# Kernel tuning notes

Hardware: AMD Instinct MI355X
Metric: run time of the kernel (lower is better)

The kernel has to match this reference:

```python
import jax, jax.numpy as jnp
import numpy as np

S, B, H = 4096, 64, 256
D = 2.0
SIGMA = D / 2.0


def setup_inputs() -> dict:
    key = jax.random.key(0)
    ks = jax.random.split(key, 7)
    return {
        "e": jax.random.normal(ks[0], (S, B, H), dtype=jnp.float32),
        "d": jax.random.normal(ks[1], (1, B, H), dtype=jnp.float32),
        "W_a": jax.random.normal(ks[2], (H, H), dtype=jnp.float32) / np.sqrt(H),
        "W_p": jax.random.normal(ks[3], (H, H), dtype=jnp.float32) / np.sqrt(H),
        "v_p": jax.random.normal(ks[4], (H, 1), dtype=jnp.float32) / np.sqrt(H),
        "lin_w": jax.random.normal(ks[5], (H, 2 * H), dtype=jnp.float32) / np.sqrt(2 * H),
        "lin_b": jax.random.normal(ks[6], (H,), dtype=jnp.float32) * 0.01,
    }


def reference(e, d, W_a, W_p, v_p, lin_w, lin_b):
    s = e.shape[0]
    # alignment: scores over source positions, softmax along S (dim 0 in torch)
    scores = jnp.sum((d @ W_a) * e, axis=2)          # [S, B]
    a = jax.nn.softmax(scores, axis=0)               # [S, B]
    # predictive position gating (Luong local-p attention)
    h = jnp.tanh(d[0] @ W_p)                         # [B, H]
    p_center = jax.nn.sigmoid((h @ v_p)[:, 0])[None, :] * s   # [1, B]
    pos = jnp.arange(s, dtype=e.dtype)[:, None]      # [S, 1]
    diff = p_center - pos                            # [S, B]
    mask = (jnp.abs(diff) <= D).astype(e.dtype)
    p = jnp.exp(-(diff * diff) / (2.0 * SIGMA * SIGMA)) * mask  # [S, B]
    w = a * p                                        # [S, B]
    context = jnp.einsum('sbh,sb->bh', e, w)[None]   # [1, B, H]
    x = jnp.concatenate([context, d], axis=2)        # [1, B, 2H]
    out = jax.nn.relu(x @ lin_w.T + lin_b)           # dropout = identity (eval)
    return out, w
```

## Files before the change

### kernel.cpp

```cpp
#include <hip/hip_runtime.h>
#include <math.h>

constexpr int S_ = 4096;
constexpr int B_ = 64;
constexpr int H_ = 256;


__global__ __launch_bounds__(256) void k1_prep(const float* __restrict__ d,
                                               const float* __restrict__ W_a,
                                               const float* __restrict__ W_p,
                                               const float* __restrict__ v_p,
                                               float* __restrict__ dW,
                                               float* __restrict__ pc) {
  int b = blockIdx.x;
  int h = threadIdx.x;
  float acc_a = 0.f, acc_p = 0.f;
  const float* db = d + b * H_;
  for (int k = 0; k < H_; ++k) {
    float dv = db[k];
    acc_a = fmaf(dv, W_a[k * H_ + h], acc_a);
    acc_p = fmaf(dv, W_p[k * H_ + h], acc_p);
  }
  dW[b * H_ + h] = acc_a;
  float prod = tanhf(acc_p) * v_p[h];
  __shared__ float red[256];
  red[h] = prod;
  __syncthreads();
  for (int st = 128; st > 0; st >>= 1) {
    if (h < st) red[h] += red[h + st];
    __syncthreads();
  }
  if (h == 0) {
    pc[b] = (float)S_ / (1.f + expf(-red[0]));
  }
}

__global__ __launch_bounds__(256) void k2_scores(const float* __restrict__ e,
                                                 const float* __restrict__ dW,
                                                 float* __restrict__ scores) {
  int b = blockIdx.x;
  int wave = threadIdx.x >> 6;
  int lane = threadIdx.x & 63;
  float4 wv = *(const float4*)(dW + b * H_ + lane * 4);
  int s_base = blockIdx.y * 64 + wave * 16;
  const float* ebase = e + (size_t)s_base * (B_ * H_) + (size_t)b * H_ + (size_t)lane * 4;
#pragma unroll 1
  for (int c = 0; c < 2; ++c) {
    float4 ev[8];
#pragma unroll
    for (int i = 0; i < 8; ++i)
      ev[i] = *(const float4*)(ebase + (size_t)(c * 8 + i) * (B_ * H_));
#pragma unroll
    for (int i = 0; i < 8; ++i) {
      float acc = fmaf(ev[i].x, wv.x, fmaf(ev[i].y, wv.y, fmaf(ev[i].z, wv.z, ev[i].w * wv.w)));
#pragma unroll
      for (int off = 32; off > 0; off >>= 1) acc += __shfl_xor(acc, off, 64);
      if (lane == 0) scores[b * S_ + s_base + c * 8 + i] = acc;
    }
  }
}

__global__ __launch_bounds__(256) void kF(const float* __restrict__ scores,
                                          const float* __restrict__ pc,
                                          const float* __restrict__ e,
                                          const float* __restrict__ d,
                                          const float* __restrict__ lin_w,
                                          const float* __restrict__ lin_b,
                                          float* __restrict__ out,
                                          float* __restrict__ w_out) {
  int b = blockIdx.x;
  int t = threadIdx.x;
  const float* sc = scores + b * S_;
  float v[16];
  float lm = -INFINITY;
#pragma unroll
  for (int k = 0; k < 16; ++k) {
    v[k] = sc[t + k * 256];
    lm = fmaxf(lm, v[k]);
  }
  __shared__ float red[256];
  red[t] = lm;
  __syncthreads();
  for (int st = 128; st > 0; st >>= 1) {
    if (t < st) red[t] = fmaxf(red[t], red[t + st]);
    __syncthreads();
  }
  float mb = red[0];
  __syncthreads();
  float ls = 0.f;
#pragma unroll
  for (int k = 0; k < 16; ++k) ls += expf(v[k] - mb);
  red[t] = ls;
  __syncthreads();
  for (int st = 128; st > 0; st >>= 1) {
    if (t < st) red[t] += red[t + st];
    __syncthreads();
  }
  float inv_l = 1.f / red[0];
  float pcb = pc[b];
#pragma unroll
  for (int k = 0; k < 16; ++k) {
    int s = t + k * 256;
    float diff = pcb - (float)s;
    float p = (fabsf(diff) <= 2.f) ? expf(-0.5f * diff * diff) : 0.f;
    w_out[(size_t)s * B_ + b] = expf(v[k] - mb) * inv_l * p;
  }
  int s0 = max(0, (int)ceilf(pcb - 2.f));
  int s1 = min(S_ - 1, (int)floorf(pcb + 2.f));
  float ctx = 0.f;
  for (int s = s0; s <= s1; ++s) {
    float diff = pcb - (float)s;
    float wv = expf(sc[s] - mb) * inv_l * expf(-0.5f * diff * diff);
    ctx = fmaf(wv, e[((size_t)s * B_ + b) * H_ + t], ctx);
  }
  __shared__ float x[512];
  x[t] = ctx;
  x[256 + t] = d[b * H_ + t];
  __syncthreads();
  float acc = lin_b[t];
  const float4* lw = (const float4*)(lin_w + t * 2 * H_);
  const float4* xv = (const float4*)x;
#pragma unroll 4
  for (int k = 0; k < 128; ++k) {
    float4 a4 = lw[k];
    float4 b4 = xv[k];
    acc += a4.x * b4.x + a4.y * b4.y + a4.z * b4.z + a4.w * b4.w;
  }
  out[b * H_ + t] = fmaxf(acc, 0.f);
}

extern "C" void kernel_launch(void* const* d_in, const int* in_sizes, int n_in,
                              void* d_out, int out_size, void* d_ws, size_t ws_size,
                              hipStream_t stream) {
  const float* e     = (const float*)d_in[0];
  const float* d     = (const float*)d_in[1];
  const float* W_a   = (const float*)d_in[2];
  const float* W_p   = (const float*)d_in[3];
  const float* v_p   = (const float*)d_in[4];
  const float* lin_w = (const float*)d_in[5];
  const float* lin_b = (const float*)d_in[6];

  float* out   = (float*)d_out;
  float* w_out = out + B_ * H_;

  float* ws     = (float*)d_ws;
  float* dW     = ws;
  float* pc     = ws + 16384;
  float* scores = ws + 16448;

  k1_prep<<<B_, 256, 0, stream>>>(d, W_a, W_p, v_p, dW, pc);
  k2_scores<<<dim3(B_, S_ / 64), 256, 0, stream>>>(e, dW, scores);
  kF<<<B_, 256, 0, stream>>>(scores, pc, e, d, lin_w, lin_b, out, w_out);
}
```

Before: 83.87 us.

## Restructure score kernel so each block covers all batches for four positions

The score kernel now assigns four threads per batch row and keeps that row's dW vector in registers. Each block handles four source positions across all 64 batches and reads contiguous slabs of e. This replaces the full 64-lane shuffle reduction per row with a 2-step reduction and coalesces score writes through a shared-memory transpose. The cost is higher register use (16 float4 of weights plus 8 float4 loads in flight) and a strided access pattern within each thread's row.

Measured after the change: 86.05 us. 2.6% more time.

```diff
diff --git a/kernel.cpp b/kernel.cpp
--- a/kernel.cpp
+++ b/kernel.cpp
@@ -38,26 +38,49 @@
 __global__ __launch_bounds__(256) void k2_scores(const float* __restrict__ e,
                                                  const float* __restrict__ dW,
                                                  float* __restrict__ scores) {
-  int b = blockIdx.x;
-  int wave = threadIdx.x >> 6;
-  int lane = threadIdx.x & 63;
-  float4 wv = *(const float4*)(dW + b * H_ + lane * 4);
-  int s_base = blockIdx.y * 64 + wave * 16;
-  const float* ebase = e + (size_t)s_base * (B_ * H_) + (size_t)b * H_ + (size_t)lane * 4;
-#pragma unroll 1
-  for (int c = 0; c < 2; ++c) {
-    float4 ev[8];
+  int t = threadIdx.x;
+  int wave = t >> 6;
+  int lane = t & 63;
+  int bl = lane >> 2;
+  int sub = lane & 3;
+  int b = wave * 16 + bl;
+  int s0 = blockIdx.x * 4;
+
+  const float4* dW4 = (const float4*)(dW + b * H_);
+  float4 wreg[16];
 #pragma unroll
-    for (int i = 0; i < 8; ++i)
-      ev[i] = *(const float4*)(ebase + (size_t)(c * 8 + i) * (B_ * H_));
+  for (int j = 0; j < 16; ++j) wreg[j] = dW4[sub + 4 * j];
+
+  float sc[4];
 #pragma unroll
-    for (int i = 0; i < 8; ++i) {
-      float acc = fmaf(ev[i].x, wv.x, fmaf(ev[i].y, wv.y, fmaf(ev[i].z, wv.z, ev[i].w * wv.w)));
+  for (int r = 0; r < 4; ++r) {
+    const float4* erow = (const float4*)(e + ((size_t)(s0 + r) * B_ + b) * H_);
+    float acc = 0.f;
 #pragma unroll
-      for (int off = 32; off > 0; off >>= 1) acc += __shfl_xor(acc, off, 64);
-      if (lane == 0) scores[b * S_ + s_base + c * 8 + i] = acc;
+    for (int half = 0; half < 2; ++half) {
+      float4 ev[8];
+#pragma unroll
+      for (int j = 0; j < 8; ++j) ev[j] = erow[sub + 4 * (half * 8 + j)];
+#pragma unroll
+      for (int j = 0; j < 8; ++j) {
+        const float4 wv = wreg[half * 8 + j];
+        acc = fmaf(ev[j].x, wv.x, fmaf(ev[j].y, wv.y,
+              fmaf(ev[j].z, wv.z, fmaf(ev[j].w, wv.w, acc))));
+      }
     }
+    acc += __shfl_xor(acc, 1, 64);
+    acc += __shfl_xor(acc, 2, 64);
+    sc[r] = acc;
   }
+
+  __shared__ float tile[4][64];
+  if (sub == 0) {
+#pragma unroll
+    for (int r = 0; r < 4; ++r) tile[r][b] = sc[r];
+  }
+  __syncthreads();
+  int b_out = t >> 2, r = t & 3;
+  scores[b_out * S_ + s0 + r] = tile[r][b_out];
 }
 
 __global__ __launch_bounds__(256) void kF(const float* __restrict__ scores,
@@ -149,6 +172,6 @@
   float* scores = ws + 16448;
 
   k1_prep<<<B_, 256, 0, stream>>>(d, W_a, W_p, v_p, dW, pc);
-  k2_scores<<<dim3(B_, S_ / 64), 256, 0, stream>>>(e, dW, scores);
+  k2_scores<<<S_ / 4, 256, 0, stream>>>(e, dW, scores);
   kF<<<B_, 256, 0, stream>>>(scores, pc, e, d, lin_w, lin_b, out, w_out);
 }
```
